# Performance work log

Hardware: AMD Instinct MI355X
Metric: run time of the kernel (lower is better)

The kernel has to match this reference:

```python
import jax, jax.numpy as jnp
import numpy as np

K_MAX = 16
SCALE = 1.0 / (32 * 32)


def setup_inputs() -> dict:
    key = jax.random.key(0)
    k1, k2, k3 = jax.random.split(key, 3)
    B, C_in, C_out, H, W = 16, 32, 32, 256, 256
    x = jax.random.normal(k1, (B, C_in, H, W), dtype=jnp.float32)
    weights_real = SCALE * jax.random.normal(k2, (C_in, C_out, K_MAX, K_MAX), dtype=jnp.float32)
    weights_imag = SCALE * jax.random.normal(k3, (C_in, C_out, K_MAX, K_MAX), dtype=jnp.float32)
    return {"x": x, "weights_real": weights_real, "weights_imag": weights_imag}


def reference(x, weights_real, weights_imag):
    B, C, H, W = x.shape
    C_out = weights_real.shape[1]
    k = min(K_MAX, H, W // 2 + 1)
    x_ft = jnp.fft.rfft2(x, norm='ortho')                 # (B, C, H, W//2+1) complex64
    w = (weights_real + 1j * weights_imag)[:, :, :k, :k]  # (C, C_out, k, k)
    # Faithful to original einsum 'bijk,ijkm->bkm' with broadcast over the
    # size-1 i/j slices: sums x_ft over its ROW axis; x_ft's COLUMN index
    # becomes the output-block row index.
    S = jnp.sum(x_ft[:, :, :k, :k], axis=2)               # (B, C, k)  indexed by freq column
    blk = jnp.einsum('bir,iorc->borc', S, w)              # (B, C_out, k, k)
    out_ft = jnp.zeros((B, C_out, H, W // 2 + 1), dtype=x_ft.dtype)
    out_ft = out_ft.at[:, :, :k, :k].set(blk)
    return jnp.fft.irfft2(out_ft, s=(H, W), norm='ortho')
```

## Files before the change

### kernel.cpp

```cpp
#include <hip/hip_runtime.h>
#include <math.h>


#define TWO_PI_OVER_256 0.02454369260617026

__global__ __launch_bounds__(256) void k1_partial(
    const float* __restrict__ x, float* __restrict__ s_part)
{
    __shared__ float twc[256], tws[256];
    __shared__ float gre[64], gim[64];
    __shared__ float Pre[4][256], Pim[4][256];
    __shared__ float red_re[16][16], red_im[16][16];

    const int t = threadIdx.x;
    const int blk = blockIdx.x;
    const int bi = blk >> 2, chunk = blk & 3;
    const int y0 = chunk << 6;

    {
        double a = TWO_PI_OVER_256 * (double)t;
        twc[t] = (float)cos(a);
        tws[t] = (float)sin(a);
    }
    __syncthreads();
    if (t < 64) {
        const int h = y0 + t;
        float gr = 0.f, gi = 0.f;
        #pragma unroll
        for (int u = 0; u < 16; ++u) {
            const int idx = (u * h) & 255;
            gr += twc[idx];
            gi -= tws[idx];
        }
        gre[t] = gr; gim[t] = gi;
    }
    __syncthreads();

    const float* img = x + (size_t)bi * 65536 + (size_t)y0 * 256;
    const int cg = t & 63, rg = t >> 6;
    float4 pr = {0.f,0.f,0.f,0.f}, pi = {0.f,0.f,0.f,0.f};
    #pragma unroll 4
    for (int k = 0; k < 16; ++k) {
        const int hl = rg + (k << 2);
        const float4 xv = *(const float4*)(img + (hl << 8) + (cg << 2));
        const float gr = gre[hl], gi = gim[hl];
        pr.x += gr * xv.x; pr.y += gr * xv.y; pr.z += gr * xv.z; pr.w += gr * xv.w;
        pi.x += gi * xv.x; pi.y += gi * xv.y; pi.z += gi * xv.z; pi.w += gi * xv.w;
    }
    *(float4*)&Pre[rg][cg << 2] = pr;
    *(float4*)&Pim[rg][cg << 2] = pi;
    __syncthreads();

    {
        const int v = t >> 4, j = t & 15;
        float ar = 0.f, ai = 0.f;
        #pragma unroll
        for (int m = 0; m < 16; ++m) {
            const int w = j + (m << 4);
            const float prr = Pre[0][w] + Pre[1][w] + Pre[2][w] + Pre[3][w];
            const float pii = Pim[0][w] + Pim[1][w] + Pim[2][w] + Pim[3][w];
            const int idx = (v * w) & 255;
            const float c = twc[idx], s = tws[idx];
            ar += prr * c + pii * s;
            ai += pii * c - prr * s;
        }
        red_re[v][j] = ar; red_im[v][j] = ai;
    }
    __syncthreads();
    if (t < 16) {
        float ar = 0.f, ai = 0.f;
        #pragma unroll
        for (int j = 0; j < 16; ++j) { ar += red_re[t][j]; ai += red_im[t][j]; }
        float* sp = s_part + (size_t)bi * 128 + chunk * 32;
        sp[t]      = ar * (1.0f / 256.0f);
        sp[t + 16] = ai * (1.0f / 256.0f);
    }
}

__global__ __launch_bounds__(256) void k23_synth(
    const float* __restrict__ wr, const float* __restrict__ wi,
    const float* __restrict__ s_part, float* __restrict__ out)
{
    __shared__ float twc[256], tws[256];
    __shared__ float Sre[32][16], Sim[32][16];
    __shared__ float Br[256], Bi[256];
    __shared__ __align__(16) float coef[64][36];

    const int t = threadIdx.x;
    const int blk = blockIdx.x;
    const int bo = blk >> 2;
    const int y0 = (blk & 3) << 6;
    const int b = bo >> 5, o = bo & 31;

    {
        double a = TWO_PI_OVER_256 * (double)t;
        twc[t] = (float)cos(a);
        tws[t] = (float)sin(a);
    }
    {
        const float* sb = s_part + (size_t)b * 4096;
        #pragma unroll
        for (int e = t; e < 512; e += 256) {
            const int i = e >> 4, u = e & 15;
            const float* p = sb + i * 128 + u;
            Sre[i][u] = p[0] + p[32] + p[64] + p[96];
            Sim[i][u] = p[16] + p[48] + p[80] + p[112];
        }
    }
    __syncthreads();

    {
        const int u = t >> 4;
        float br = 0.f, bim = 0.f;
        const float* wrp = wr + o * 256 + t;
        const float* wip = wi + o * 256 + t;
        #pragma unroll 8
        for (int i = 0; i < 32; ++i) {
            const float a_re = Sre[i][u], a_im = Sim[i][u];
            const float w_re = wrp[i * 8192], w_im = wip[i * 8192];
            br  += a_re * w_re - a_im * w_im;
            bim += a_re * w_im + a_im * w_re;
        }
        Br[t] = br; Bi[t] = bim;
    }
    __syncthreads();

    {
        const int v = t & 15, slot = t >> 4;
        float br[16], bim[16];
        #pragma unroll
        for (int u = 0; u < 16; ++u) { br[u] = Br[u * 16 + v]; bim[u] = Bi[u * 16 + v]; }
        const float scale = (v == 0) ? (1.0f / 256.0f) : (1.0f / 128.0f);
        #pragma unroll
        for (int m = 0; m < 4; ++m) {
            const int r = slot * 4 + m;
            const int y = y0 + r;
            const float c1 = twc[y], s1 = tws[y];
            float gr = br[0], gi = bim[0];
            float cc = 1.f, cs = 0.f;
            #pragma unroll
            for (int u = 1; u < 16; ++u) {
                const float nc = cc * c1 - cs * s1;
                const float ns = cc * s1 + cs * c1;
                cc = nc; cs = ns;
                gr += br[u] * cc - bim[u] * cs;
                gi += br[u] * cs + bim[u] * cc;
            }
            coef[r][v]      = gr * scale;
            coef[r][16 + v] = (v == 0) ? 0.f : (-gi * scale);
        }
    }
    __syncthreads();

    float c[16], s[16];
    #pragma unroll
    for (int v = 0; v < 16; ++v) {
        const int idx = (v * t) & 255;
        c[v] = twc[idx];
        s[v] = tws[idx];
    }
    s[0] = 0.f;

    float* op = out + (size_t)bo * 65536 + (size_t)y0 * 256 + t;
    #pragma unroll 2
    for (int r = 0; r < 64; ++r) {
        const float4* crow = (const float4*)&coef[r][0];
        float acc = 0.f;
        #pragma unroll
        for (int q = 0; q < 4; ++q) {
            const float4 pc = crow[q];
            acc += pc.x * c[q*4+0] + pc.y * c[q*4+1] + pc.z * c[q*4+2] + pc.w * c[q*4+3];
        }
        #pragma unroll
        for (int q = 0; q < 4; ++q) {
            const float4 ps = crow[4+q];
            acc += ps.x * s[q*4+0] + ps.y * s[q*4+1] + ps.z * s[q*4+2] + ps.w * s[q*4+3];
        }
        op[r * 256] = acc;
    }
}

extern "C" void kernel_launch(void* const* d_in, const int* in_sizes, int n_in,
                              void* d_out, int out_size, void* d_ws, size_t ws_size,
                              hipStream_t stream) {
    (void)in_sizes; (void)n_in; (void)out_size; (void)ws_size;
    const float* x  = (const float*)d_in[0];
    const float* wr = (const float*)d_in[1];
    const float* wi = (const float*)d_in[2];
    float* out    = (float*)d_out;
    float* s_part = (float*)d_ws;

    k1_partial<<<2048, 256, 0, stream>>>(x, s_part);
    k23_synth<<<2048, 256, 0, stream>>>(wr, wi, s_part, out);
}
```

Before: 279.2 us.

## Split synthesis into coefficient and output kernels; use float sincosf twiddles

The fused synth kernel recomputed the channel contraction (weights × S) in every one of four row-chunk blocks per (b,o). It is now split: a 512-block kernel computes all 256 row coefficients once per (b,o) into a global workspace, and a separate kernel reads them to synthesize output rows. Double-precision cos/sin twiddle setup is replaced by float sincosf. The cost is an extra launch plus a global round trip of the coefficients (about 16 MB written and read). The synth loop now reads coefficients from global memory with scalar loads instead of LDS float4 loads.

```diff
diff --git a/kernel.cpp b/kernel.cpp
--- a/kernel.cpp
+++ b/kernel.cpp
@@ -2,7 +2,7 @@
 #include <math.h>
 
 
-#define TWO_PI_OVER_256 0.02454369260617026
+#define TWO_PI_OVER_256 0.02454369260617026f
 
 __global__ __launch_bounds__(256) void k1_partial(
     const float* __restrict__ x, float* __restrict__ s_part)
@@ -18,9 +18,9 @@
     const int y0 = chunk << 6;
 
     {
-        double a = TWO_PI_OVER_256 * (double)t;
-        twc[t] = (float)cos(a);
-        tws[t] = (float)sin(a);
+        float sv, cv;
+        sincosf(TWO_PI_OVER_256 * (float)t, &sv, &cv);
+        twc[t] = cv; tws[t] = sv;
     }
     __syncthreads();
     if (t < 64) {
@@ -77,25 +77,22 @@
     }
 }
 
-__global__ __launch_bounds__(256) void k23_synth(
+__global__ __launch_bounds__(256) void k2_coef(
     const float* __restrict__ wr, const float* __restrict__ wi,
-    const float* __restrict__ s_part, float* __restrict__ out)
+    const float* __restrict__ s_part, float* __restrict__ coef)
 {
     __shared__ float twc[256], tws[256];
     __shared__ float Sre[32][16], Sim[32][16];
     __shared__ float Br[256], Bi[256];
-    __shared__ __align__(16) float coef[64][36];
 
     const int t = threadIdx.x;
-    const int blk = blockIdx.x;
-    const int bo = blk >> 2;
-    const int y0 = (blk & 3) << 6;
+    const int bo = blockIdx.x;
     const int b = bo >> 5, o = bo & 31;
 
     {
-        double a = TWO_PI_OVER_256 * (double)t;
-        twc[t] = (float)cos(a);
-        tws[t] = (float)sin(a);
+        float sv, cv;
+        sincosf(TWO_PI_OVER_256 * (float)t, &sv, &cv);
+        twc[t] = cv; tws[t] = sv;
     }
     {
         const float* sb = s_part + (size_t)b * 4096;
@@ -126,15 +123,13 @@
     __syncthreads();
 
     {
-        const int v = t & 15, slot = t >> 4;
+        const int v = t & 15, yg = t >> 4;
         float br[16], bim[16];
         #pragma unroll
         for (int u = 0; u < 16; ++u) { br[u] = Br[u * 16 + v]; bim[u] = Bi[u * 16 + v]; }
         const float scale = (v == 0) ? (1.0f / 256.0f) : (1.0f / 128.0f);
-        #pragma unroll
-        for (int m = 0; m < 4; ++m) {
-            const int r = slot * 4 + m;
-            const int y = y0 + r;
+        for (int m = 0; m < 16; ++m) {
+            const int y = yg * 16 + m;
             const float c1 = twc[y], s1 = tws[y];
             float gr = br[0], gi = bim[0];
             float cc = 1.f, cs = 0.f;
@@ -146,9 +141,26 @@
                 gr += br[u] * cc - bim[u] * cs;
                 gi += br[u] * cs + bim[u] * cc;
             }
-            coef[r][v]      = gr * scale;
-            coef[r][16 + v] = (v == 0) ? 0.f : (-gi * scale);
-        }
+            float* cp = coef + (((size_t)bo * 256 + y) << 5);
+            cp[v]      = gr * scale;
+            cp[16 + v] = (v == 0) ? 0.f : (-gi * scale);
+        }
+    }
+}
+
+__global__ __launch_bounds__(256) void k3_synth(
+    const float* __restrict__ coef, float* __restrict__ out)
+{
+    __shared__ float twc[256], tws[256];
+    const int t = threadIdx.x;
+    const int blk = blockIdx.x;
+    const int bo = blk >> 2;
+    const int y0 = (blk & 3) << 6;
+
+    {
+        float sv, cv;
+        sincosf(TWO_PI_OVER_256 * (float)t, &sv, &cv);
+        twc[t] = cv; tws[t] = sv;
     }
     __syncthreads();
 
@@ -161,20 +173,15 @@
     }
     s[0] = 0.f;
 
+    const float* cp = coef + ((size_t)bo * 256 + y0) * 32;
     float* op = out + (size_t)bo * 65536 + (size_t)y0 * 256 + t;
-    #pragma unroll 2
     for (int r = 0; r < 64; ++r) {
-        const float4* crow = (const float4*)&coef[r][0];
+        const float* p = cp + r * 32;
         float acc = 0.f;
         #pragma unroll
-        for (int q = 0; q < 4; ++q) {
-            const float4 pc = crow[q];
-            acc += pc.x * c[q*4+0] + pc.y * c[q*4+1] + pc.z * c[q*4+2] + pc.w * c[q*4+3];
-        }
-        #pragma unroll
-        for (int q = 0; q < 4; ++q) {
-            const float4 ps = crow[4+q];
-            acc += ps.x * s[q*4+0] + ps.y * s[q*4+1] + ps.z * s[q*4+2] + ps.w * s[q*4+3];
+        for (int v = 0; v < 16; ++v) {
+            acc += p[v] * c[v];
+            acc += p[v + 16] * s[v];
         }
         op[r * 256] = acc;
     }
@@ -189,7 +196,9 @@
     const float* wi = (const float*)d_in[2];
     float* out    = (float*)d_out;
     float* s_part = (float*)d_ws;
+    float* coef   = s_part + 65536;
 
     k1_partial<<<2048, 256, 0, stream>>>(x, s_part);
-    k23_synth<<<2048, 256, 0, stream>>>(wr, wi, s_part, out);
-}
+    k2_coef<<<512, 256, 0, stream>>>(wr, wi, s_part, coef);
+    k3_synth<<<2048, 256, 0, stream>>>(coef, out);
+}
```

Result: no change. 281.6 us (+0.9%).
